# Optimization experiments

Hardware: AMD Instinct MI355X
Metric: run time of the kernel (lower is better)

The kernel has to match this reference:

```python
import jax, jax.numpy as jnp
import numpy as np
from jax import lax

N, C, H, W = 16, 1, 512, 512
MAX_ITERS = H + W  # upper bound on flood-fill propagation distance


def _dilate4(r):
    # 3x3 cross (4-connectivity) grayscale dilation, r: (N,H,W)
    rp = jnp.pad(r, ((0, 0), (1, 1), (1, 1)))
    up = rp[:, :-2, 1:-1]
    dn = rp[:, 2:, 1:-1]
    lf = rp[:, 1:-1, :-2]
    rt = rp[:, 1:-1, 2:]
    return jnp.maximum(jnp.maximum(jnp.maximum(up, dn), jnp.maximum(lf, rt)), r)


def _reconstruct_dilation(marker, mask):
    # skimage.morphology.reconstruction(seed, mask, method='dilation'):
    # iterate rec = min(dilate(rec), mask) until convergence.
    def cond(state):
        _, changed, i = state
        return jnp.logical_and(changed, i < MAX_ITERS)

    def body(state):
        r, _, i = state
        nr = jnp.minimum(_dilate4(r), mask)
        return nr, jnp.any(nr != r), i + 1

    rec, _, _ = lax.while_loop(cond, body, (marker, jnp.array(True), jnp.array(0)))
    return rec


def _adaptive_binarize(prob, marker_factor, mask_factor):
    # prob: (N,1,H,W); mirrors torch .detach() -> threshold -> reconstruction
    img = lax.stop_gradient(prob[:, 0])  # (N,H,W)
    nzm = img > 0
    cnt = jnp.sum(nzm, axis=(1, 2))                      # (N,)
    safe = jnp.maximum(cnt, 1).astype(img.dtype)
    mean = jnp.sum(jnp.where(nzm, img, 0.0), axis=(1, 2)) / safe
    var = jnp.sum(jnp.where(nzm, (img - mean[:, None, None]) ** 2, 0.0), axis=(1, 2)) / safe
    std = jnp.sqrt(var)

    def threshold(factor):
        T = (mean + factor * std)[:, None, None]
        b = img > T
        empty = jnp.sum(b, axis=(1, 2)) == 0
        T2 = (mean + (factor / 2.0) * std)[:, None, None]
        b2 = img > T2
        return jnp.where(empty[:, None, None], b2, b)

    marker = threshold(marker_factor).astype(jnp.float32)
    maskb = threshold(mask_factor).astype(jnp.float32)
    rec = _reconstruct_dilation(marker, maskb)
    out = (rec > 0.5).astype(jnp.float32)
    out = jnp.where((cnt == 0)[:, None, None], 0.0, out)  # no nonzero pixels -> zeros
    return out[:, None]  # (N,1,H,W)


def setup_inputs() -> dict:
    key = jax.random.key(0)
    k1, k2 = jax.random.split(key)
    thick_logit = jax.random.normal(k1, (N, C, H, W), dtype=jnp.float32)
    thin_logit = jax.random.normal(k2, (N, C, H, W), dtype=jnp.float32)
    return {"thick_logit": thick_logit, "thin_logit": thin_logit}


def reference(thick_logit, thin_logit):
    thick_prob = jax.nn.sigmoid(thick_logit)
    thin_prob = jax.nn.sigmoid(thin_logit)
    thick_bin = _adaptive_binarize(thick_prob, 2.0, 0.5)
    thin_bin = _adaptive_binarize(thin_prob, 4.0, 0.5)
    fused_bin = jnp.clip(thick_bin + thin_bin, 0.0, 1.0)
    return thick_logit, thin_logit, fused_bin
```

## Files before the change

kernel.cpp:

```cpp
#include <hip/hip_runtime.h>
#include <cstdint>
#include <cstddef>

#define HW 512
#define NPIX (HW * HW)
#define NIMG 16
#define NII 32
#define CHUNKS 64
#define CHUNK_PIX 4096
#define IN_ELEMS (NIMG * NPIX)
#define WPI 4096

typedef unsigned long long u64;

#define WS_PARTA 0u
#define WS_ZM    65536u
#define WS_MSEL  98304u
#define WS_KSEL  (WS_MSEL + 1048576u)
#define WS_ROUT  (WS_KSEL + 1048576u)

__device__ __forceinline__ float sigmoid_f32(float x) {
    return (float)(1.0 / (1.0 + exp(-(double)x)));
}

__device__ __forceinline__ float sigmoid_fast(float xf) {
    double x = (double)xf;
    double y = x * -1.4426950408889634074;
    if (y > 1000.0)  return 0.0f;
    if (y < -1000.0) return 1.0f;
    double n = __builtin_rint(y);
    double t = (y - n) * 0.69314718055994530942;
    double p = 2.5052108385441718775e-8;
    p = __builtin_fma(p, t, 2.7557319223985890653e-7);
    p = __builtin_fma(p, t, 2.7557319223985892511e-6);
    p = __builtin_fma(p, t, 2.4801587301587301566e-5);
    p = __builtin_fma(p, t, 1.9841269841269841253e-4);
    p = __builtin_fma(p, t, 1.3888888888888889419e-3);
    p = __builtin_fma(p, t, 8.3333333333333332177e-3);
    p = __builtin_fma(p, t, 4.1666666666666664354e-2);
    p = __builtin_fma(p, t, 1.6666666666666665741e-1);
    p = __builtin_fma(p, t, 5.0e-1);
    p = __builtin_fma(p, t, 1.0);
    p = __builtin_fma(p, t, 1.0);
    long long bits = ((long long)n + 1023ll) << 52;
    double e = p * __longlong_as_double(bits);
    double d = 1.0 + e;
    if (y > 100.0 || y < -100.0)
        return (float)(1.0 / d);
    double r = (double)__builtin_amdgcn_rcpf((float)d);
    r = r * (2.0 - d * r);
    r = r * (2.0 - d * r);
    return (float)r;
}

__global__ void k1_copy_stats(const float* __restrict__ A, const float* __restrict__ B,
                              float* __restrict__ out, double* __restrict__ partA) {
    int b = blockIdx.x;
    int ii = b >> 6, chunk = b & 63;
    int j = ii >> 4, n = ii & 15;
    const float* src = (j == 0 ? A : B) + (size_t)n * NPIX + (size_t)chunk * CHUNK_PIX;
    float* dst = out + (size_t)j * IN_ELEMS + (size_t)n * NPIX + (size_t)chunk * CHUNK_PIX;

    double s = 0.0, sq = 0.0, cc = 0.0;
    float mx = -__builtin_inff();
#pragma unroll
    for (int p = 0; p < 4; ++p) {
        float4 v = *(const float4*)(src + p * 1024 + threadIdx.x * 4);
        *(float4*)(dst + p * 1024 + threadIdx.x * 4) = v;
        float xs[4] = {v.x, v.y, v.z, v.w};
#pragma unroll
        for (int q = 0; q < 4; ++q) {
            float img = sigmoid_fast(xs[q]);
            mx = fmaxf(mx, xs[q]);
            if (img > 0.0f) { double d = (double)img; s += d; sq += d * d; cc += 1.0; }
        }
    }
    __shared__ double sm[256], sv[256], sc[256];
    __shared__ float smx[256];
    sm[threadIdx.x] = s; sv[threadIdx.x] = sq; sc[threadIdx.x] = cc; smx[threadIdx.x] = mx;
    __syncthreads();
    for (int off = 128; off > 0; off >>= 1) {
        if (threadIdx.x < off) {
            sm[threadIdx.x] += sm[threadIdx.x + off];
            sv[threadIdx.x] += sv[threadIdx.x + off];
            sc[threadIdx.x] += sc[threadIdx.x + off];
            smx[threadIdx.x] = fmaxf(smx[threadIdx.x], smx[threadIdx.x + off]);
        }
        __syncthreads();
    }
    if (threadIdx.x == 0) {
        double* p = partA + (size_t)(ii * 64 + chunk) * 4;
        p[0] = sm[0]; p[1] = sv[0]; p[2] = sc[0]; p[3] = (double)smx[0];
    }
}

__device__ __forceinline__ float key_to_f32(unsigned k) {
    unsigned b = (k & 0x80000000u) ? (k ^ 0x80000000u) : ~k;
    return __uint_as_float(b);
}
__device__ float find_cut(double T) {
    if (!(1.0 > T)) return __uint_as_float(0x7F800000u);
    unsigned lo = 0x007FFFFFu;
    unsigned hi = 0xFF800000u;
    while (lo < hi) {
        unsigned mid = lo + ((hi - lo) >> 1);
        float x = key_to_f32(mid);
        float s32 = sigmoid_f32(x);
        if ((double)s32 > T) hi = mid; else lo = mid + 1;
    }
    return key_to_f32(lo);
}

__global__ void k2_bits(const float* __restrict__ A, const float* __restrict__ B,
                        const double* __restrict__ partA,
                        u64* __restrict__ msel, u64* __restrict__ ksel,
                        u64* __restrict__ zm) {
    int b = blockIdx.x, ii = b >> 6, chunk = b & 63;
    int j = ii >> 4, n = ii & 15;
    const float* src = (j == 0 ? A : B) + (size_t)n * NPIX;
    int t = threadIdx.x, lane = t & 63, w = t >> 6;

    __shared__ double shst[4];
    __shared__ float cs[4];
    __shared__ float cut2[2];

    if (t < 64) {
        const double* p = partA + (size_t)(ii * 64 + t) * 4;
        double s = p[0], sq = p[1], c = p[2], mx = p[3];
#pragma unroll
        for (int off = 32; off > 0; off >>= 1) {
            s  += __shfl_down(s,  (unsigned)off, 64);
            sq += __shfl_down(sq, (unsigned)off, 64);
            c  += __shfl_down(c,  (unsigned)off, 64);
            mx  = fmax(mx, __shfl_down(mx, (unsigned)off, 64));
        }
        if (t == 0) {
            double mean = 0.0, sd = 0.0;
            if (c > 0.0) {
                mean = s / c;
                double var = sq / c - mean * mean;
                if (var < 0.0) var = 0.0;
                sd = sqrt(var);
            }
            shst[0] = mean; shst[1] = sd; shst[2] = c; shst[3] = mx;
        }
    }
    __syncthreads();
    if (t < 4) {
        double mean = shst[0], sd = shst[1];
        double fac = (ii < 16) ? 2.0 : 4.0;
        double T = (t == 0) ? mean + fac * sd
                 : (t == 1) ? mean + 0.5 * fac * sd
                 : (t == 2) ? mean + 0.5 * sd
                 :            mean + 0.25 * sd;
        cs[t] = find_cut(T);
    }
    __syncthreads();
    if (t == 0) {
        float mxf = (float)shst[3];
        cut2[0] = (mxf >= cs[0]) ? cs[0] : cs[1];
        cut2[1] = (mxf >= cs[2]) ? cs[2] : cs[3];
        if (chunk == 0) zm[ii] = (shst[2] > 0.0) ? ~0ull : 0ull;
    }
    __syncthreads();
    float cM = cut2[0], cK = cut2[1];

#pragma unroll 4
    for (int i = 0; i < 16; ++i) {
        float x = src[chunk * CHUNK_PIX + i * 256 + t];
        u64 bM = __ballot(x >= cM);
        u64 bK = __ballot(x >= cK);
        if (lane == 0) {
            size_t g = (size_t)ii * WPI + (size_t)chunk * 64 + i * 4 + w;
            msel[g] = bM; ksel[g] = bK;
        }
    }
}

__device__ __forceinline__ void hfill8(u64* x, const u64* k) {
    u64 c = 0;
#pragma unroll
    for (int w = 0; w < 8; ++w) {
        u64 a = k[w], g = x[w];
        u64 t1 = a + g;  u64 c1 = (u64)(t1 < a);
        u64 t2 = t1 + c; u64 c2 = (u64)(t2 < t1);
        c = c1 | c2;
        x[w] = (~t2 | g) & a;
    }
    c = 0;
#pragma unroll
    for (int w = 7; w >= 0; --w) {
        u64 a = __brevll(k[w]), g = __brevll(x[w]);
        u64 t1 = a + g;  u64 c1 = (u64)(t1 < a);
        u64 t2 = t1 + c; u64 c2 = (u64)(t2 < t1);
        c = c1 | c2;
        x[w] = __brevll((~t2 | g) & a);
    }
}

__global__ __launch_bounds__(512) void k3_flood(const u64* __restrict__ msel,
                                                const u64* __restrict__ ksel,
                                                u64* __restrict__ rout) {
    int ii = blockIdx.x, t = threadIdx.x;
    __shared__ u64 R[8 * HW];
    const u64* M = msel + (size_t)ii * WPI;
    const u64* K = ksel + (size_t)ii * WPI;

    u64 r[8], k[8];
#pragma unroll
    for (int w = 0; w < 8; ++w) {
        k[w] = K[(size_t)t * 8 + w];
        r[w] = M[(size_t)t * 8 + w] & k[w];
    }
    hfill8(r, k);
#pragma unroll
    for (int w = 0; w < 8; ++w) R[w * HW + t] = r[w];
    __syncthreads();

    for (int round = 0; round < 256; ++round) {
        u64 gained = 0;
#pragma unroll 1
        for (int sweep = 0; sweep < 4; ++sweep) {
            u64 diff = 0;
#pragma unroll
            for (int w = 0; w < 8; ++w) {
                u64 nb = (t > 0      ? R[w * HW + (t - 1)] : 0ull)
                       | (t < HW - 1 ? R[w * HW + (t + 1)] : 0ull);
                u64 g = nb & k[w] & ~r[w];
                r[w] |= g; diff |= g;
            }
            if (diff) {
                hfill8(r, k);
#pragma unroll
                for (int w = 0; w < 8; ++w) R[w * HW + t] = r[w];
                gained |= diff;
            }
            asm volatile("" ::: "memory");
        }
        if (!__syncthreads_or(gained != 0ull ? 1 : 0)) break;
    }

#pragma unroll
    for (int w = 0; w < 8; ++w)
        rout[(size_t)ii * WPI + (size_t)w * HW + t] = r[w];
}

__global__ void k4_fuse(const u64* __restrict__ rout,
                        const u64* __restrict__ zm,
                        float* __restrict__ out) {
    size_t gid = (size_t)blockIdx.x * blockDim.x + threadIdx.x;
    size_t p = gid * 4;
    int n = (int)(p >> 18);
    int e = (int)(p & (NPIX - 1));
    size_t gw = (size_t)(((e >> 6) & 7) * HW + (e >> 9));
    u64 w = (rout[(size_t)n * WPI + gw] & zm[n])
          | (rout[(size_t)(16 + n) * WPI + gw] & zm[16 + n]);
    int sh = e & 63;
    float4 v;
    v.x = ((w >> sh) & 1ull)       ? 1.0f : 0.0f;
    v.y = ((w >> (sh + 1)) & 1ull) ? 1.0f : 0.0f;
    v.z = ((w >> (sh + 2)) & 1ull) ? 1.0f : 0.0f;
    v.w = ((w >> (sh + 3)) & 1ull) ? 1.0f : 0.0f;
    *(float4*)(out + 2 * (size_t)IN_ELEMS + p) = v;
}

extern "C" void kernel_launch(void* const* d_in, const int* in_sizes, int n_in,
                              void* d_out, int out_size, void* d_ws, size_t ws_size,
                              hipStream_t stream) {
    const float* A = (const float*)d_in[0];
    const float* B = (const float*)d_in[1];
    float* out = (float*)d_out;
    char* ws = (char*)d_ws;

    double* partA = (double*)(ws + WS_PARTA);
    u64*    zm    = (u64*)(ws + WS_ZM);
    u64*    msel  = (u64*)(ws + WS_MSEL);
    u64*    ksel  = (u64*)(ws + WS_KSEL);
    u64*    rout  = (u64*)(ws + WS_ROUT);

    k1_copy_stats<<<NII * CHUNKS, 256, 0, stream>>>(A, B, out, partA);
    k2_bits<<<NII * CHUNKS, 256, 0, stream>>>(A, B, partA, msel, ksel, zm);
    k3_flood<<<NII, 512, 0, stream>>>(msel, ksel, rout);
    k4_fuse<<<4096, 256, 0, stream>>>(rout, zm, out);
}
```

Measured before the change: 142.7 us.

## Replace vertical neighbor sweeps with bit-transposed horizontal fills

The flood-fill kernel now transposes the 512x512 bit image in shared memory with a wavefront-shuffle bit transpose. This lets vertical propagation reuse the carry-based full-row fill (hfill8), so each cycle alternates a full horizontal fill and a full vertical fill. It is meant to cut the number of rounds, since the old version advanced vertically only one row per sweep. In exchange each cycle pays for two 512x512 bit transposes and extra barriers, uses 1024 threads of which half sit idle during fills, and doubles shared memory use.

Measured after the change: 181.2 us. 27.0% more time.

```diff
diff --git a/kernel.cpp b/kernel.cpp
--- a/kernel.cpp
+++ b/kernel.cpp
@@ -198,51 +198,106 @@
     }
 }
 
-__global__ __launch_bounds__(512) void k3_flood(const u64* __restrict__ msel,
-                                                const u64* __restrict__ ksel,
-                                                u64* __restrict__ rout) {
+#define XSTAGE(jc, mc) {                                     \
+    u64 p  = __shfl_xor(x, jc, 64);                          \
+    u64 lo = (L & jc) ? p : x;        \
+    u64 hi = (L & jc) ? x : p;        \
+    u64 tt = ((lo >> jc) ^ hi) & mc;                         \
+    x ^= (L & jc) ? tt : (tt << jc); }
+
+__device__ __forceinline__ void xpose512(const u64* __restrict__ S,
+                                         u64* __restrict__ D,
+                                         int L, int I, int J0) {
+#pragma unroll
+    for (int jj = 0; jj < 4; ++jj) {
+        int J = J0 + jj;
+        u64 x = S[J * 512 + I * 64 + L];
+        XSTAGE(32, 0x00000000FFFFFFFFull)
+        XSTAGE(16, 0x0000FFFF0000FFFFull)
+        XSTAGE(8,  0x00FF00FF00FF00FFull)
+        XSTAGE(4,  0x0F0F0F0F0F0F0F0Full)
+        XSTAGE(2,  0x3333333333333333ull)
+        XSTAGE(1,  0x5555555555555555ull)
+        D[I * 512 + J * 64 + L] = x;
+    }
+}
+
+__global__ __launch_bounds__(1024) void k3_hv(const u64* __restrict__ msel,
+                                              const u64* __restrict__ ksel,
+                                              u64* __restrict__ rout) {
+    __shared__ u64 Rb[8 * HW];
+    __shared__ u64 Tb[8 * HW];
     int ii = blockIdx.x, t = threadIdx.x;
-    __shared__ u64 R[8 * HW];
+    int L = t & 63, W = t >> 6;
+    int I = W >> 1, J0 = (W & 1) * 4;
     const u64* M = msel + (size_t)ii * WPI;
     const u64* K = ksel + (size_t)ii * WPI;
 
-    u64 r[8], k[8];
-#pragma unroll
-    for (int w = 0; w < 8; ++w) {
-        k[w] = K[(size_t)t * 8 + w];
-        r[w] = M[(size_t)t * 8 + w] & k[w];
-    }
-    hfill8(r, k);
-#pragma unroll
-    for (int w = 0; w < 8; ++w) R[w * HW + t] = r[w];
-    __syncthreads();
-
-    for (int round = 0; round < 256; ++round) {
-        u64 gained = 0;
-#pragma unroll 1
-        for (int sweep = 0; sweep < 4; ++sweep) {
-            u64 diff = 0;
-#pragma unroll
-            for (int w = 0; w < 8; ++w) {
-                u64 nb = (t > 0      ? R[w * HW + (t - 1)] : 0ull)
-                       | (t < HW - 1 ? R[w * HW + (t + 1)] : 0ull);
-                u64 g = nb & k[w] & ~r[w];
-                r[w] |= g; diff |= g;
+    u64 k8[8], kT8[8], r8[8];
+    if (t < HW) {
+#pragma unroll
+        for (int w = 0; w < 8; ++w) {
+            k8[w] = K[(size_t)t * 8 + w];
+            r8[w] = M[(size_t)t * 8 + w] & k8[w];
+        }
+        hfill8(r8, k8);
+#pragma unroll
+        for (int w = 0; w < 8; ++w) Rb[w * HW + t] = k8[w];
+    }
+    __syncthreads();
+    xpose512(Rb, Tb, L, I, J0);
+    __syncthreads();
+    if (t < HW) {
+#pragma unroll
+        for (int w = 0; w < 8; ++w) kT8[w] = Tb[w * HW + t];
+#pragma unroll
+        for (int w = 0; w < 8; ++w) Rb[w * HW + t] = r8[w];
+    }
+    __syncthreads();
+
+    for (int cyc = 0; cyc < 200; ++cyc) {
+        xpose512(Rb, Tb, L, I, J0);
+        __syncthreads();
+        u64 d = 0;
+        if (t < HW) {
+            u64 x8[8], o8[8];
+#pragma unroll
+            for (int w = 0; w < 8; ++w) { x8[w] = Tb[w * HW + t]; o8[w] = x8[w]; }
+            hfill8(x8, kT8);
+            u64 dd = 0;
+#pragma unroll
+            for (int w = 0; w < 8; ++w) dd |= x8[w] ^ o8[w];
+            if (dd) {
+#pragma unroll
+                for (int w = 0; w < 8; ++w) Tb[w * HW + t] = x8[w];
             }
-            if (diff) {
-                hfill8(r, k);
-#pragma unroll
-                for (int w = 0; w < 8; ++w) R[w * HW + t] = r[w];
-                gained |= diff;
+            d |= dd;
+        }
+        __syncthreads();
+        xpose512(Tb, Rb, L, I, J0);
+        __syncthreads();
+        if (t < HW) {
+            u64 x8[8], o8[8];
+#pragma unroll
+            for (int w = 0; w < 8; ++w) { x8[w] = Rb[w * HW + t]; o8[w] = x8[w]; }
+            hfill8(x8, k8);
+            u64 dd = 0;
+#pragma unroll
+            for (int w = 0; w < 8; ++w) dd |= x8[w] ^ o8[w];
+            if (dd) {
+#pragma unroll
+                for (int w = 0; w < 8; ++w) Rb[w * HW + t] = x8[w];
             }
-            asm volatile("" ::: "memory");
-        }
-        if (!__syncthreads_or(gained != 0ull ? 1 : 0)) break;
-    }
-
-#pragma unroll
-    for (int w = 0; w < 8; ++w)
-        rout[(size_t)ii * WPI + (size_t)w * HW + t] = r[w];
+            d |= dd;
+        }
+        if (!__syncthreads_or(d != 0ull ? 1 : 0)) break;
+    }
+
+    if (t < HW) {
+#pragma unroll
+        for (int w = 0; w < 8; ++w)
+            rout[(size_t)ii * WPI + (size_t)w * HW + t] = Rb[w * HW + t];
+    }
 }
 
 __global__ void k4_fuse(const u64* __restrict__ rout,
@@ -280,6 +335,6 @@
 
     k1_copy_stats<<<NII * CHUNKS, 256, 0, stream>>>(A, B, out, partA);
     k2_bits<<<NII * CHUNKS, 256, 0, stream>>>(A, B, partA, msel, ksel, zm);
-    k3_flood<<<NII, 512, 0, stream>>>(msel, ksel, rout);
+    k3_hv<<<NII, 1024, 0, stream>>>(msel, ksel, rout);
     k4_fuse<<<4096, 256, 0, stream>>>(rout, zm, out);
 }
```

## Replace shared-memory row sweeps with wavefront shuffle-based vertical flood fill

Applied to the files above, without the earlier changes.

The flood-fill kernel now propagates vertically inside each 64-row wavefront using log-step shuffle-up/down scans, iterating until the wavefront is stable. Only the boundary rows of each wavefront are exchanged through small shared arrays between block-wide syncs. This is meant to cut the number of block barriers and shared-memory row traffic compared with the old per-row neighbor sweeps. In exchange each stabilization pass costs many shuffles and can loop up to 32 times per round.

Measured after the change: 179.5 us. 25.8% more time.

```diff
diff --git a/kernel.cpp b/kernel.cpp
--- a/kernel.cpp
+++ b/kernel.cpp
@@ -198,11 +198,54 @@
     }
 }
 
+__device__ __forceinline__ u64 shu64(u64 x, int d, int lane) {
+    u64 y = __shfl_up(x, (unsigned)d, 64);
+    return (lane >= d) ? y : 0ull;
+}
+__device__ __forceinline__ u64 shd64(u64 x, int d, int lane) {
+    u64 y = __shfl_down(x, (unsigned)d, 64);
+    return (lane + d <= 63) ? y : 0ull;
+}
+
+__device__ __forceinline__ u64 vstab(u64 (&r)[8], const u64 (&k)[8], int lane, bool& redo) {
+    u64 total = 0;
+    bool more;
+    int it = 0;
+    do {
+        u64 vdiff = 0;
+#pragma unroll
+        for (int w = 0; w < 8; ++w) {
+            u64 o = k[w];
+            u64 v = r[w], ok = o, sv, so;
+            v |= shu64(v, 1, lane) & ok;
+            sv = shu64(v, 1, lane); so = shu64(ok, 1, lane); v |= sv & ok; ok &= so;
+            sv = shu64(v, 2, lane); so = shu64(ok, 2, lane); v |= sv & ok; ok &= so;
+            v |= shu64(v, 4, lane) & ok;
+            u64 dn = v;
+            v = r[w]; ok = o;
+            v |= shd64(v, 1, lane) & ok;
+            sv = shd64(v, 1, lane); so = shd64(ok, 1, lane); v |= sv & ok; ok &= so;
+            sv = shd64(v, 2, lane); so = shd64(ok, 2, lane); v |= sv & ok; ok &= so;
+            v |= shd64(v, 4, lane) & ok;
+            u64 nw = dn | v;
+            vdiff |= nw ^ r[w];
+            r[w] = nw;
+        }
+        if (vdiff) hfill8(r, k);
+        total |= vdiff;
+        more = (__any((int)(vdiff != 0ull)) != 0);
+    } while (more && ++it < 32);
+    redo = more;
+    return total;
+}
+
 __global__ __launch_bounds__(512) void k3_flood(const u64* __restrict__ msel,
                                                 const u64* __restrict__ ksel,
                                                 u64* __restrict__ rout) {
     int ii = blockIdx.x, t = threadIdx.x;
-    __shared__ u64 R[8 * HW];
+    int lane = t & 63, wv = t >> 6;
+    __shared__ u64 Btop[8][8];
+    __shared__ u64 Bbot[8][8];
     const u64* M = msel + (size_t)ii * WPI;
     const u64* K = ksel + (size_t)ii * WPI;
 
@@ -213,31 +256,47 @@
         r[w] = M[(size_t)t * 8 + w] & k[w];
     }
     hfill8(r, k);
-#pragma unroll
-    for (int w = 0; w < 8; ++w) R[w * HW + t] = r[w];
+    bool redo;
+    vstab(r, k, lane, redo);
+    if (lane == 0) {
+#pragma unroll
+        for (int w = 0; w < 8; ++w) Btop[wv][w] = r[w];
+    }
+    if (lane == 63) {
+#pragma unroll
+        for (int w = 0; w < 8; ++w) Bbot[wv][w] = r[w];
+    }
     __syncthreads();
 
     for (int round = 0; round < 256; ++round) {
-        u64 gained = 0;
-#pragma unroll 1
-        for (int sweep = 0; sweep < 4; ++sweep) {
-            u64 diff = 0;
+        u64 g = 0;
+        if (lane == 0 && wv > 0) {
 #pragma unroll
             for (int w = 0; w < 8; ++w) {
-                u64 nb = (t > 0      ? R[w * HW + (t - 1)] : 0ull)
-                       | (t < HW - 1 ? R[w * HW + (t + 1)] : 0ull);
-                u64 g = nb & k[w] & ~r[w];
-                r[w] |= g; diff |= g;
-            }
-            if (diff) {
-                hfill8(r, k);
-#pragma unroll
-                for (int w = 0; w < 8; ++w) R[w * HW + t] = r[w];
-                gained |= diff;
-            }
-            asm volatile("" ::: "memory");
-        }
-        if (!__syncthreads_or(gained != 0ull ? 1 : 0)) break;
+                u64 a = Bbot[wv - 1][w] & k[w] & ~r[w];
+                r[w] |= a; g |= a;
+            }
+        } else if (lane == 63 && wv < 7) {
+#pragma unroll
+            for (int w = 0; w < 8; ++w) {
+                u64 a = Btop[wv + 1][w] & k[w] & ~r[w];
+                r[w] |= a; g |= a;
+            }
+        }
+        if (g) hfill8(r, k);
+        u64 tot = 0;
+        if (__any((int)((g != 0ull) || redo))) {
+            tot = vstab(r, k, lane, redo);
+            if (lane == 0) {
+#pragma unroll
+                for (int w = 0; w < 8; ++w) Btop[wv][w] = r[w];
+            }
+            if (lane == 63) {
+#pragma unroll
+                for (int w = 0; w < 8; ++w) Bbot[wv][w] = r[w];
+            }
+        }
+        if (!__syncthreads_or((int)(((g | tot) != 0ull) || redo))) break;
     }
 
 #pragma unroll
```
